# Kernel tuning notes

Measured on AMD Instinct MI355X. Metric: run time of the kernel, lower is better.

## Reference

```python
import jax, jax.numpy as jnp
import numpy as np

N, E, F, ED, L = 50000, 800000, 64, 16, 2
EPS_BN = 1e-5


def setup_inputs() -> dict:
    key = jax.random.key(0)
    ks = jax.random.split(key, 8)
    s = 0.05
    return {
        "x": jax.random.normal(ks[0], (N, F), jnp.float32),
        "edge_index": jax.random.randint(ks[1], (2, E), 0, N),
        "edge_attr": jax.random.normal(ks[2], (E, ED), jnp.float32),
        # per-layer stacked params (L layers)
        "We": jax.random.normal(ks[3], (L, ED, F), jnp.float32) * s,
        "be": jnp.zeros((L, F), jnp.float32),
        "Wpre": jax.random.normal(ks[4], (L, 2 * F, F), jnp.float32) * s,
        "bpre": jnp.zeros((L, F), jnp.float32),
        "Wpost": jax.random.normal(ks[5], (L, 7 * F, F), jnp.float32) * s,
        "bpost": jnp.zeros((L, F), jnp.float32),
        "Wlin": jax.random.normal(ks[6], (L, F, F), jnp.float32) * s,
        "blin": jnp.zeros((L, F), jnp.float32),
        "gamma": jnp.ones((L, F), jnp.float32),
        "beta": jnp.zeros((L, F), jnp.float32),
    }


def _layer(x, src, dst, edge_attr, We, be, Wpre, bpre, Wpost, bpost, Wlin, blin, gamma, beta):
    # message: edge encoder + pre-MLP on cat(x_j, e)   [E, F]
    e = edge_attr @ We + be
    h = jnp.concatenate([x[src], e], axis=-1) @ Wpre + bpre
    # multi-aggregator segment reduce to target nodes (index = dst)
    cnt = jax.ops.segment_sum(jnp.ones(h.shape[0], h.dtype), dst, num_segments=N)
    safe_cnt = jnp.maximum(cnt, 1.0)
    mean = jax.ops.segment_sum(h, dst, num_segments=N) / safe_cnt[:, None]
    empty = (cnt == 0)[:, None]
    mn = jnp.where(empty, 0.0, jax.ops.segment_min(h, dst, num_segments=N))
    mx = jnp.where(empty, 0.0, jax.ops.segment_max(h, dst, num_segments=N))
    agg = jnp.concatenate([mean, mn, mx], axis=-1)  # [N, 3F]
    # scalers: identity, then amplification (deg=None => avg from bincount of degrees)
    deg_i = cnt.astype(jnp.int32)
    bc = jnp.bincount(deg_i, length=N).astype(h.dtype)
    avg_log = jnp.mean(jnp.log(bc + 1.0))
    amp = (jnp.log(safe_cnt + 1.0) / avg_log)[:, None]
    out = jnp.concatenate([agg, agg * amp], axis=-1)  # [N, 6F]
    # post-MLP on cat(x, aggregated), final linear
    out = jnp.concatenate([x, out], axis=-1) @ Wpost + bpost  # [N, F]
    out = out @ Wlin + blin
    # BatchNorm1d (batch stats, biased var) + ReLU
    mu = out.mean(axis=0)
    var = jnp.mean((out - mu) ** 2, axis=0)
    out = gamma * (out - mu) / jnp.sqrt(var + EPS_BN) + beta
    return jax.nn.relu(out)


def reference(x, edge_index, edge_attr, We, be, Wpre, bpre, Wpost, bpost, Wlin, blin, gamma, beta):
    src, dst = edge_index[0], edge_index[1]
    for l in range(L):
        x = _layer(x, src, dst, edge_attr, We[l], be[l], Wpre[l], bpre[l],
                   Wpost[l], bpost[l], Wlin[l], blin[l], gamma[l], beta[l])
    return x
```

## Files before the change

kernel.cpp:

```cpp
#include <hip/hip_runtime.h>
#include <math.h>

static constexpr int NN = 50000;
static constexpr long NE = 800000;
static constexpr int FF = 64;
static constexpr int EDIM = 16;
static constexpr int NLAYER = 2;
static constexpr float EPSBN = 1e-5f;
static constexpr int NGRP = NN / 16;
static constexpr int SCB = 512;
static constexpr int NSCB = (NN + SCB - 1) / SCB;
static constexpr int LDSW = 68;

typedef __attribute__((ext_vector_type(8))) short short8v;
typedef __attribute__((ext_vector_type(4))) float f32x4;

#define MFMA16(a, b, c) __builtin_amdgcn_mfma_f32_16x16x32_bf16(a, b, c, 0, 0, 0)

__device__ __forceinline__ short f2bf(float f) {
    unsigned u = __float_as_uint(f);
    unsigned r = u + 0x7FFFu + ((u >> 16) & 1u);
    return (short)(r >> 16);
}
__device__ __forceinline__ float bf2f(unsigned short h) {
    return __uint_as_float(((unsigned)h) << 16);
}
__device__ __forceinline__ unsigned pk2(float lo, float hi) {
    return (unsigned)(unsigned short)f2bf(lo) | ((unsigned)(unsigned short)f2bf(hi) << 16);
}
__device__ __forceinline__ short8v pack8(const float* p) {
    const float4* q = (const float4*)p;
    float4 a = q[0], b = q[1];
    short8v v;
    v[0] = f2bf(a.x); v[1] = f2bf(a.y); v[2] = f2bf(a.z); v[3] = f2bf(a.w);
    v[4] = f2bf(b.x); v[5] = f2bf(b.y); v[6] = f2bf(b.z); v[7] = f2bf(b.w);
    return v;
}
__device__ __forceinline__ short8v pack8bn(const float* p, const float* sc, int f0) {
    const float4* q = (const float4*)p;
    float4 a = q[0], b = q[1];
    float v[8] = {a.x, a.y, a.z, a.w, b.x, b.y, b.z, b.w};
    short8v r;
#pragma unroll
    for (int j = 0; j < 8; ++j) {
        float y = fmaxf(fmaf(v[j], sc[f0 + j], sc[FF + f0 + j]), 0.f);
        r[j] = f2bf(y);
    }
    return r;
}
__device__ __forceinline__ void pack8s(const float* p, short8v& hi, short8v& lo) {
    const float4* q = (const float4*)p;
    float4 a = q[0], b = q[1];
    float v[8] = {a.x, a.y, a.z, a.w, b.x, b.y, b.z, b.w};
#pragma unroll
    for (int j = 0; j < 8; ++j) {
        short h = f2bf(v[j]);
        hi[j] = h;
        lo[j] = f2bf(v[j] - bf2f((unsigned short)h));
    }
}
__device__ __forceinline__ void pack8s_bn(const float* p, const float* sc, int f0,
                                          short8v& hi, short8v& lo) {
    const float4* q = (const float4*)p;
    float4 a = q[0], b = q[1];
    float v[8] = {a.x, a.y, a.z, a.w, b.x, b.y, b.z, b.w};
#pragma unroll
    for (int j = 0; j < 8; ++j) {
        float y = fmaxf(fmaf(v[j], sc[f0 + j], sc[FF + f0 + j]), 0.f);
        short h = f2bf(y);
        hi[j] = h;
        lo[j] = f2bf(y - bf2f((unsigned short)h));
    }
}
__device__ __forceinline__ void pack8fs(const float* v, short8v& hi, short8v& lo) {
#pragma unroll
    for (int j = 0; j < 8; ++j) {
        short h = f2bf(v[j]);
        hi[j] = h;
        lo[j] = f2bf(v[j] - bf2f((unsigned short)h));
    }
}

__global__ void fold_kernel(const float* __restrict__ We, const float* __restrict__ be,
                            const float* __restrict__ Wpre, const float* __restrict__ bpre,
                            const float* __restrict__ Wpost, const float* __restrict__ bpost,
                            const float* __restrict__ Wlin, const float* __restrict__ blin,
                            float* __restrict__ Weff, float* __restrict__ beff,
                            float* __restrict__ Wc, float* __restrict__ cfold) {
    int l = blockIdx.x >> 4;
    int s = blockIdx.x & 15;
    int t = threadIdx.x;
    const float* We_l    = We    + l * EDIM * FF;
    const float* Wpre_e  = Wpre  + l * 2 * FF * FF + FF * FF;
    const float* Wpost_l = Wpost + l * 7 * FF * FF;
    const float* Wlin_l  = Wlin  + l * FF * FF;

    __shared__ float slin[FF * FF];
    __shared__ float spre[FF * FF];
    for (int i = t; i < FF * FF; i += blockDim.x) { slin[i] = Wlin_l[i]; spre[i] = Wpre_e[i]; }
    __syncthreads();

    for (int i = s * 256 + t; i < EDIM * FF; i += 16 * 256) {
        int j = i >> 6, f = i & 63;
        float a = 0.f;
        for (int k = 0; k < FF; ++k) a += We_l[j * FF + k] * spre[k * FF + f];
        Weff[l * EDIM * FF + i] = a;
    }
    for (int i = s * 256 + t; i < FF; i += 16 * 256) {
        float a = bpre[l * FF + i];
        for (int k = 0; k < FF; ++k) a += be[l * FF + k] * spre[k * FF + i];
        beff[l * FF + i] = a;
    }
    for (int i = s * 256 + t; i < 7 * FF * FF; i += 16 * 256) {
        int r = i >> 6, f = i & 63;
        float a = 0.f;
        for (int k = 0; k < FF; ++k) a += Wpost_l[r * FF + k] * slin[k * FF + f];
        Wc[l * 7 * FF * FF + i] = a;
    }
    for (int i = s * 256 + t; i < FF; i += 16 * 256) {
        float a = blin[l * FF + i];
        for (int k = 0; k < FF; ++k) a += bpost[l * FF + k] * slin[k * FF + i];
        cfold[l * FF + i] = a;
    }
}

__global__ void fragify_all(const float* __restrict__ Wpre, const float* __restrict__ Weff,
                            const float* __restrict__ Wc,
                            short* __restrict__ WpreF, short* __restrict__ WeffF,
                            short* __restrict__ WcFh, short* __restrict__ WcFl) {
    int b = blockIdx.x;
    int l = b / 17, r = b % 17;
    int t = threadIdx.x;
    const float* src; short* dh; short* dl = nullptr; int kc, Kreal;
    if (r < 2)      { src = Wpre + (size_t)l * 2 * FF * FF; dh = WpreF + l * 4096;  kc = r;     Kreal = 64; }
    else if (r < 3) { src = Weff + (size_t)l * EDIM * FF;   dh = WeffF + l * 2048;  kc = 0;     Kreal = 16; }
    else            { src = Wc   + (size_t)l * 7 * FF * FF; dh = WcFh + l * 28672;
                      dl = WcFl + l * 28672;                                        kc = r - 3; Kreal = 448; }
    int idx = kc * 256 + t;
    int lane = idx & 63, nt = (idx >> 6) & 3;
    int m = lane & 15, kh = lane >> 4;
    short8v hv, lv;
#pragma unroll
    for (int j = 0; j < 8; ++j) {
        int k = kc * 32 + kh * 8 + j;
        float val = (k < Kreal) ? src[k * FF + nt * 16 + m] : 0.f;
        short h = f2bf(val);
        hv[j] = h;
        lv[j] = f2bf(val - bf2f((unsigned short)h));
    }
    ((short8v*)dh)[idx] = hv;
    if (dl) ((short8v*)dl)[idx] = lv;
}


__global__ void build_zero(int* __restrict__ rowcnt, int* __restrict__ fill,
                           int* __restrict__ bc, float* __restrict__ avglog) {
    long i = (long)blockIdx.x * 256 + threadIdx.x;
    long stride = (long)gridDim.x * 256;
    for (long j = i; j < NN; j += stride) { rowcnt[j] = 0; fill[j] = 0; bc[j] = 0; }
    if (i == 0) avglog[0] = 0.f;
}

__global__ void hist_dst(const int* __restrict__ ei, int* __restrict__ rowcnt) {
    long e = (long)blockIdx.x * 256 + threadIdx.x;
    if (e < NE) atomicAdd(&rowcnt[ei[NE + e]], 1);
}

__global__ void scan_a(const int* __restrict__ rowcnt, int* __restrict__ part) {
    __shared__ int red[SCB];
    int t = threadIdx.x;
    int i = blockIdx.x * SCB + t;
    red[t] = (i < NN) ? rowcnt[i] : 0;
    __syncthreads();
    for (int o = SCB / 2; o > 0; o >>= 1) {
        if (t < o) red[t] += red[t + o];
        __syncthreads();
    }
    if (t == 0) part[blockIdx.x] = red[0];
}

__global__ void scan_b(int* __restrict__ part, int* __restrict__ rowptr) {
    __shared__ int s[128];
    int t = threadIdx.x;
    int v = (t < NSCB) ? part[t] : 0;
    s[t] = v;
    __syncthreads();
    for (int o = 1; o < 128; o <<= 1) {
        int u = (t >= o) ? s[t - o] : 0;
        __syncthreads();
        s[t] += u;
        __syncthreads();
    }
    if (t < NSCB) part[t] = s[t] - v;
    if (t == 127) rowptr[NN] = s[127];
}

__global__ void scan_c(const int* __restrict__ rowcnt, const int* __restrict__ part,
                       int* __restrict__ rowptr) {
    __shared__ int s[SCB];
    int t = threadIdx.x;
    int i = blockIdx.x * SCB + t;
    int v = (i < NN) ? rowcnt[i] : 0;
    s[t] = v;
    __syncthreads();
    for (int o = 1; o < SCB; o <<= 1) {
        int u = (t >= o) ? s[t - o] : 0;
        __syncthreads();
        s[t] += u;
        __syncthreads();
    }
    if (i < NN) rowptr[i] = part[blockIdx.x] + s[t] - v;
}

__global__ void scatter_perm(const int* __restrict__ ei, const int* __restrict__ rowptr,
                             int* __restrict__ fill, int2* __restrict__ srcperm) {
    long e = (long)blockIdx.x * 256 + threadIdx.x;
    if (e >= NE) return;
    int d = ei[NE + e];
    int p = rowptr[d] + atomicAdd(&fill[d], 1);
    srcperm[p] = make_int2(ei[e], (int)e);
}

__global__ void gather_attr(const int2* __restrict__ srcperm, const float* __restrict__ attr,
                            int* __restrict__ srcp, short* __restrict__ attrb) {
    long p = (long)blockIdx.x * 256 + threadIdx.x;
    if (p >= NE) return;
    int2 sp = srcperm[p];
    srcp[p] = sp.x;
    long e = sp.y;
    const float4* a4 = (const float4*)(attr + e * EDIM);
    float4 A = a4[0], B = a4[1], C = a4[2], D = a4[3];
    uint4 w0, w1;
    w0.x = pk2(A.x, A.y); w0.y = pk2(A.z, A.w); w0.z = pk2(B.x, B.y); w0.w = pk2(B.z, B.w);
    w1.x = pk2(C.x, C.y); w1.y = pk2(C.z, C.w); w1.z = pk2(D.x, D.y); w1.w = pk2(D.z, D.w);
    uint4* dst = (uint4*)(attrb + p * EDIM);
    dst[0] = w0; dst[1] = w1;
}

__global__ void degbc2(const int* __restrict__ rowcnt, int* __restrict__ bc) {
    __shared__ int h[256];
    int t = threadIdx.x;
    h[t] = 0;
    __syncthreads();
    for (long n = (long)blockIdx.x * 256 + t; n < NN; n += (long)gridDim.x * 256) {
        int d = rowcnt[n];
        if (d < 256) {
            atomicAdd(&h[d], 1);
        } else {
            if (d >= NN) d = NN - 1;
            atomicAdd(&bc[d], 1);
        }
    }
    __syncthreads();
    int v = h[t];
    if (v) atomicAdd(&bc[t], v);
}

__global__ void avglog_kernel(const int* __restrict__ bc, float* __restrict__ total) {
    float s = 0.f;
    for (long i = (long)blockIdx.x * 256 + threadIdx.x; i < NN; i += (long)gridDim.x * 256)
        s += logf((float)bc[i] + 1.f);
    for (int o = 32; o; o >>= 1) s += __shfl_down(s, o, 64);
    __shared__ float wsum[4];
    int lane = threadIdx.x & 63, wid = threadIdx.x >> 6;
    if (lane == 0) wsum[wid] = s;
    __syncthreads();
    if (threadIdx.x == 0) atomicAdd(total, wsum[0] + wsum[1] + wsum[2] + wsum[3]);
}

__global__ void amp_kernel(const int* __restrict__ cnt, const float* __restrict__ total,
                           float* __restrict__ amp) {
    long n = (long)blockIdx.x * 256 + threadIdx.x;
    if (n < NN) {
        float avg = total[0] / (float)NN;
        float sc = fmaxf((float)cnt[n], 1.f);
        amp[n] = logf(sc + 1.f) / avg;
    }
}


__global__ __launch_bounds__(256) void xp_mfma(const float* __restrict__ xin,
                                               const float* __restrict__ bnsc,
                                               const short* __restrict__ WF,
                                               short* __restrict__ xpb,
                                               float* __restrict__ bnsum,
                                               float* __restrict__ bnsum2) {
    int t = threadIdx.x;
    if (blockIdx.x == 0 && t < FF) { bnsum[t] = 0.f; bnsum2[t] = 0.f; }
    int g = blockIdx.x * 4 + (t >> 6);
    if (g >= NGRP) return;
    int lane = t & 63, m = lane & 15, kh = lane >> 4;
    const float* xr = xin + (long)(g * 16 + m) * FF;
    short8v a0, a1;
    if (bnsc) {
        a0 = pack8bn(xr + kh * 8, bnsc, kh * 8);
        a1 = pack8bn(xr + 32 + kh * 8, bnsc, 32 + kh * 8);
    } else {
        a0 = pack8(xr + kh * 8);
        a1 = pack8(xr + 32 + kh * 8);
    }
    const short8v* BF = (const short8v*)WF;
    f32x4 acc[4];
#pragma unroll
    for (int nt = 0; nt < 4; ++nt) {
        f32x4 z = {0.f, 0.f, 0.f, 0.f};
        z = MFMA16(a0, BF[(0 * 4 + nt) * 64 + lane], z);
        z = MFMA16(a1, BF[(1 * 4 + nt) * 64 + lane], z);
        acc[nt] = z;
    }
#pragma unroll
    for (int nt = 0; nt < 4; ++nt)
#pragma unroll
        for (int r = 0; r < 4; ++r) {
            long node = g * 16 + kh * 4 + r;
            xpb[node * FF + nt * 16 + m] = f2bf(acc[nt][r]);
        }
}

__global__ __launch_bounds__(256) void agg_fused(
    const int* __restrict__ rowptr, const int* __restrict__ srcp,
    const short* __restrict__ attrb, const short* __restrict__ WF,
    const float* __restrict__ beff_l, const short* __restrict__ xpb,
    float* __restrict__ meanb, float* __restrict__ mnb, float* __restrict__ mxb) {
    __shared__ float eph[4][16 * LDSW];
    int t = threadIdx.x;
    int wid = t >> 6, lane = t & 63;
    int m = lane & 15, kh = lane >> 4;
    int n = blockIdx.x * 4 + wid;
    if (n >= NN) return;
    float* lds = &eph[wid][0];
    const short8v* BF = (const short8v*)WF;
    float bfv[4];
#pragma unroll
    for (int nt = 0; nt < 4; ++nt) bfv[nt] = beff_l[nt * 16 + m];
    long r0 = rowptr[n], r1 = rowptr[n + 1];
    const float INF = __builtin_huge_valf();
    float sm = 0.f, mn = INF, mx = -INF;
    const unsigned short* xu = (const unsigned short*)xpb;

    for (long base = r0; base < r1; base += 16) {
        int cnt = (int)(((r1 - base) < 16) ? (r1 - base) : 16);
        long ea = base + m; if (ea > NE - 1) ea = NE - 1;
        short8v a;
        if (kh < 2) {
            a = *(const short8v*)(attrb + ea * EDIM + kh * 8);
        } else {
#pragma unroll
            for (int j = 0; j < 8; ++j) a[j] = 0;
        }
        f32x4 ac0, ac1, ac2, ac3;
        {
            f32x4 z = {0.f, 0.f, 0.f, 0.f};
            ac0 = MFMA16(a, BF[0 * 64 + lane], z);
            ac1 = MFMA16(a, BF[1 * 64 + lane], z);
            ac2 = MFMA16(a, BF[2 * 64 + lane], z);
            ac3 = MFMA16(a, BF[3 * 64 + lane], z);
        }
#pragma unroll
        for (int r = 0; r < 4; ++r) {
            lds[(kh * 4 + r) * LDSW + 0 * 16 + m] = ac0[r] + bfv[0];
            lds[(kh * 4 + r) * LDSW + 1 * 16 + m] = ac1[r] + bfv[1];
            lds[(kh * 4 + r) * LDSW + 2 * 16 + m] = ac2[r] + bfv[2];
            lds[(kh * 4 + r) * LDSW + 3 * 16 + m] = ac3[r] + bfv[3];
        }
        int sv = srcp[base + (lane < cnt ? lane : cnt - 1)];
        int j = 0;
        for (; j + 8 <= cnt; j += 8) {
            int s0 = __shfl(sv, j + 0), s1 = __shfl(sv, j + 1);
            int s2 = __shfl(sv, j + 2), s3 = __shfl(sv, j + 3);
            int s4 = __shfl(sv, j + 4), s5 = __shfl(sv, j + 5);
            int s6 = __shfl(sv, j + 6), s7 = __shfl(sv, j + 7);
            float x0 = bf2f(xu[(long)s0 * FF + lane]);
            float x1 = bf2f(xu[(long)s1 * FF + lane]);
            float x2 = bf2f(xu[(long)s2 * FF + lane]);
            float x3 = bf2f(xu[(long)s3 * FF + lane]);
            float x4 = bf2f(xu[(long)s4 * FF + lane]);
            float x5 = bf2f(xu[(long)s5 * FF + lane]);
            float x6 = bf2f(xu[(long)s6 * FF + lane]);
            float x7 = bf2f(xu[(long)s7 * FF + lane]);
            float h0 = x0 + lds[(j + 0) * LDSW + lane];
            float h1 = x1 + lds[(j + 1) * LDSW + lane];
            float h2 = x2 + lds[(j + 2) * LDSW + lane];
            float h3 = x3 + lds[(j + 3) * LDSW + lane];
            float h4 = x4 + lds[(j + 4) * LDSW + lane];
            float h5 = x5 + lds[(j + 5) * LDSW + lane];
            float h6 = x6 + lds[(j + 6) * LDSW + lane];
            float h7 = x7 + lds[(j + 7) * LDSW + lane];
            sm += ((h0 + h1) + (h2 + h3)) + ((h4 + h5) + (h6 + h7));
            mn = fminf(mn, fminf(fminf(fminf(h0, h1), fminf(h2, h3)),
                                 fminf(fminf(h4, h5), fminf(h6, h7))));
            mx = fmaxf(mx, fmaxf(fmaxf(fmaxf(h0, h1), fmaxf(h2, h3)),
                                 fmaxf(fmaxf(h4, h5), fmaxf(h6, h7))));
        }
        for (; j < cnt; ++j) {
            int s0 = __shfl(sv, j);
            float h = bf2f(xu[(long)s0 * FF + lane]) + lds[j * LDSW + lane];
            sm += h;
            mn = fminf(mn, h);
            mx = fmaxf(mx, h);
        }
    }
    int deg = (int)(r1 - r0);
    float inv = (deg > 0) ? (1.f / (float)deg) : 0.f;
    if (deg == 0) { mn = 0.f; mx = 0.f; }
    long o = (long)n * FF + lane;
    meanb[o] = sm * inv; mnb[o] = mn; mxb[o] = mx;
}

__global__ __launch_bounds__(256, 2) void node_mfma(
    const float* __restrict__ xin, const float* __restrict__ bnsc,
    const float* __restrict__ meanb, const float* __restrict__ mnb,
    const float* __restrict__ mxb, const float* __restrict__ amp,
    const short* __restrict__ WFh, const short* __restrict__ WFl,
    const float* __restrict__ cfold_l,
    float* __restrict__ out_pre, float* __restrict__ bnsum, float* __restrict__ bnsum2) {
    __shared__ float sS[FF], sQ[FF];
    int t = threadIdx.x;
    if (t < FF) { sS[t] = 0.f; sQ[t] = 0.f; }
    __syncthreads();
    int g = blockIdx.x * 4 + (t >> 6);
    bool act = (g < NGRP);
    int lane = t & 63, m = lane & 15, kh = lane >> 4;
    if (act) {
        long n = g * 16 + m;
        float av = amp[n];
        const float* xr = xin + n * FF;
        float vme[16], vmn[16], vmx[16], sc16[16];
        {
            const float4* s4a = (const float4*)(meanb + n * FF + kh * 8);
            const float4* s4b = (const float4*)(meanb + n * FF + 32 + kh * 8);
            float4 a = s4a[0], b = s4a[1], c = s4b[0], d = s4b[1];
            vme[0]=a.x; vme[1]=a.y; vme[2]=a.z; vme[3]=a.w;
            vme[4]=b.x; vme[5]=b.y; vme[6]=b.z; vme[7]=b.w;
            vme[8]=c.x; vme[9]=c.y; vme[10]=c.z; vme[11]=c.w;
            vme[12]=d.x; vme[13]=d.y; vme[14]=d.z; vme[15]=d.w;
        }
        {
            const float4* s4a = (const float4*)(mnb + n * FF + kh * 8);
            const float4* s4b = (const float4*)(mnb + n * FF + 32 + kh * 8);
            float4 a = s4a[0], b = s4a[1], c = s4b[0], d = s4b[1];
            vmn[0]=a.x; vmn[1]=a.y; vmn[2]=a.z; vmn[3]=a.w;
            vmn[4]=b.x; vmn[5]=b.y; vmn[6]=b.z; vmn[7]=b.w;
            vmn[8]=c.x; vmn[9]=c.y; vmn[10]=c.z; vmn[11]=c.w;
            vmn[12]=d.x; vmn[13]=d.y; vmn[14]=d.z; vmn[15]=d.w;
        }
        {
            const float4* s4a = (const float4*)(mxb + n * FF + kh * 8);
            const float4* s4b = (const float4*)(mxb + n * FF + 32 + kh * 8);
            float4 a = s4a[0], b = s4a[1], c = s4b[0], d = s4b[1];
            vmx[0]=a.x; vmx[1]=a.y; vmx[2]=a.z; vmx[3]=a.w;
            vmx[4]=b.x; vmx[5]=b.y; vmx[6]=b.z; vmx[7]=b.w;
            vmx[8]=c.x; vmx[9]=c.y; vmx[10]=c.z; vmx[11]=c.w;
            vmx[12]=d.x; vmx[13]=d.y; vmx[14]=d.z; vmx[15]=d.w;
        }
        const short8v* BH = (const short8v*)WFh;
        const short8v* BL = (const short8v*)WFl;
        f32x4 accA[4], accB[4];
#pragma unroll
        for (int nt = 0; nt < 4; ++nt) {
            f32x4 z = {0.f, 0.f, 0.f, 0.f};
            accA[nt] = z; accB[nt] = z;
        }
        short8v hv, lv;
#define DO_KC3(kc, ACC) { \
        _Pragma("unroll") for (int nt = 0; nt < 4; ++nt) { \
            ACC[nt] = MFMA16(hv, BH[((kc) * 4 + nt) * 64 + lane], ACC[nt]); \
            ACC[nt] = MFMA16(lv, BH[((kc) * 4 + nt) * 64 + lane], ACC[nt]); \
            ACC[nt] = MFMA16(hv, BL[((kc) * 4 + nt) * 64 + lane], ACC[nt]); } }
        if (bnsc) {
            pack8s_bn(xr + kh * 8, bnsc, kh * 8, hv, lv);           DO_KC3(0, accA)
            pack8s_bn(xr + 32 + kh * 8, bnsc, 32 + kh * 8, hv, lv); DO_KC3(1, accB)
        } else {
            pack8s(xr + kh * 8, hv, lv);        DO_KC3(0, accA)
            pack8s(xr + 32 + kh * 8, hv, lv);   DO_KC3(1, accB)
        }
        pack8fs(vme + 0, hv, lv);           DO_KC3(2, accA)
        pack8fs(vme + 8, hv, lv);           DO_KC3(3, accB)
        pack8fs(vmn + 0, hv, lv);           DO_KC3(4, accA)
        pack8fs(vmn + 8, hv, lv);           DO_KC3(5, accB)
        pack8fs(vmx + 0, hv, lv);           DO_KC3(6, accA)
        pack8fs(vmx + 8, hv, lv);           DO_KC3(7, accB)
#pragma unroll
        for (int j = 0; j < 16; ++j) sc16[j] = vme[j] * av;
        pack8fs(sc16 + 0, hv, lv);          DO_KC3(8, accA)
        pack8fs(sc16 + 8, hv, lv);          DO_KC3(9, accB)
#pragma unroll
        for (int j = 0; j < 16; ++j) sc16[j] = vmn[j] * av;
        pack8fs(sc16 + 0, hv, lv);          DO_KC3(10, accA)
        pack8fs(sc16 + 8, hv, lv);          DO_KC3(11, accB)
#pragma unroll
        for (int j = 0; j < 16; ++j) sc16[j] = vmx[j] * av;
        pack8fs(sc16 + 0, hv, lv);          DO_KC3(12, accA)
        pack8fs(sc16 + 8, hv, lv);          DO_KC3(13, accB)
#undef DO_KC3
        float cfv[4];
#pragma unroll
        for (int nt = 0; nt < 4; ++nt) cfv[nt] = cfold_l[nt * 16 + m];
#pragma unroll
        for (int nt = 0; nt < 4; ++nt) {
            float ps = 0.f, pq = 0.f;
#pragma unroll
            for (int r = 0; r < 4; ++r) {
                float v = accA[nt][r] + accB[nt][r] + cfv[nt];
                out_pre[(long)(g * 16 + kh * 4 + r) * FF + nt * 16 + m] = v;
                ps += v;
                pq += v * v;
            }
            atomicAdd(&sS[nt * 16 + m], ps);
            atomicAdd(&sQ[nt * 16 + m], pq);
        }
    }
    __syncthreads();
    if (t < FF) {
        atomicAdd(&bnsum[t], sS[t]);
        atomicAdd(&bnsum2[t], sQ[t]);
    }
}

__global__ void bn_final(const float* __restrict__ bnsum, const float* __restrict__ bnsum2,
                         const float* __restrict__ gamma_l, const float* __restrict__ beta_l,
                         float* __restrict__ sc_sh) {
    int f = threadIdx.x;
    if (f < FF) {
        float mu = bnsum[f] / (float)NN;
        float var = bnsum2[f] / (float)NN - mu * mu;
        var = fmaxf(var, 0.f);
        float s = gamma_l[f] * rsqrtf(var + EPSBN);
        sc_sh[f] = s;
        sc_sh[FF + f] = beta_l[f] - mu * s;
    }
}

__global__ void bn_apply2(const float* __restrict__ out_pre,
                          const float* __restrict__ bnsum, const float* __restrict__ bnsum2,
                          const float* __restrict__ gamma_l, const float* __restrict__ beta_l,
                          float* __restrict__ xout) {
    int f = threadIdx.x & 63;
    float mu = bnsum[f] / (float)NN;
    float var = bnsum2[f] / (float)NN - mu * mu;
    var = fmaxf(var, 0.f);
    float s = gamma_l[f] * rsqrtf(var + EPSBN);
    float o = beta_l[f] - mu * s;
    long i = (long)blockIdx.x * 256 + threadIdx.x;
    long stride = (long)gridDim.x * 256;
    for (long j = i; j < (long)NN * FF; j += stride) {
        xout[j] = fmaxf(fmaf(out_pre[j], s, o), 0.f);
    }
}

extern "C" void kernel_launch(void* const* d_in, const int* in_sizes, int n_in,
                              void* d_out, int out_size, void* d_ws, size_t ws_size,
                              hipStream_t stream) {
    const float* x0    = (const float*)d_in[0];
    const int*   ei    = (const int*)d_in[1];
    const float* attr  = (const float*)d_in[2];
    const float* We    = (const float*)d_in[3];
    const float* be    = (const float*)d_in[4];
    const float* Wpre  = (const float*)d_in[5];
    const float* bpre  = (const float*)d_in[6];
    const float* Wpost = (const float*)d_in[7];
    const float* bpost = (const float*)d_in[8];
    const float* Wlin  = (const float*)d_in[9];
    const float* blin  = (const float*)d_in[10];
    const float* gamma = (const float*)d_in[11];
    const float* beta  = (const float*)d_in[12];
    float* out = (float*)d_out;

    char* ws = (char*)d_ws;
    size_t off = 0;
    auto carve = [&](size_t bytes) -> void* {
        void* p = ws + off;
        off += (bytes + 255) & ~(size_t)255;
        return p;
    };
    const size_t NFb = (size_t)NN * FF * 4;
    float*    Weff   = (float*)carve(2 * EDIM * FF * 4);
    float*    beff   = (float*)carve(2 * FF * 4);
    float*    Wc     = (float*)carve(2 * 7 * FF * FF * 4);
    float*    cfold  = (float*)carve(2 * FF * 4);
    short*    WpreF  = (short*)carve(2 * 4096 * 2);
    short*    WeffF  = (short*)carve(2 * 2048 * 2);
    short*    WcFh   = (short*)carve(2 * 28672 * 2);
    short*    WcFl   = (short*)carve(2 * 28672 * 2);
    int*      srcp   = (int*)carve(NE * 4);
    short*    attrb  = (short*)carve((size_t)NE * EDIM * 2);
    int*      rowptr = (int*)carve((NN + 1) * 4);
    int*      rowcnt = (int*)carve(NN * 4);
    int*      fill   = (int*)carve(NN * 4);
    int*      bc     = (int*)carve(NN * 4);
    float*    amp    = (float*)carve(NN * 4);
    int*      part   = (int*)carve(NSCB * 4);
    short*    xpb    = (short*)carve((size_t)NN * FF * 2);
    float*    meanb  = (float*)carve(NFb);
    float*    mnb    = (float*)carve(NFb);
    float*    mxb    = (float*)carve(NFb);
    float*    preA   = (float*)carve(NFb);
    float*    preB   = (float*)carve(NFb);
    float*    bnsum  = (float*)carve(FF * 4);
    float*    bnsum2 = (float*)carve(FF * 4);
    float*    avglog = (float*)carve(4);
    float*    sc_sh  = (float*)carve(2 * FF * 4);
    int2*     srcperm = (int2*)preB;

    const int EB = (int)((NE + 255) / 256);

    build_zero<<<196, 256, 0, stream>>>(rowcnt, fill, bc, avglog);
    hist_dst<<<EB, 256, 0, stream>>>(ei, rowcnt);
    scan_a<<<NSCB, SCB, 0, stream>>>(rowcnt, part);
    scan_b<<<1, 128, 0, stream>>>(part, rowptr);
    scan_c<<<NSCB, SCB, 0, stream>>>(rowcnt, part, rowptr);
    scatter_perm<<<EB, 256, 0, stream>>>(ei, rowptr, fill, srcperm);
    gather_attr<<<EB, 256, 0, stream>>>(srcperm, attr, srcp, attrb);
    degbc2<<<196, 256, 0, stream>>>(rowcnt, bc);
    avglog_kernel<<<128, 256, 0, stream>>>(bc, avglog);
    amp_kernel<<<196, 256, 0, stream>>>(rowcnt, avglog, amp);
    fold_kernel<<<32, 256, 0, stream>>>(We, be, Wpre, bpre, Wpost, bpost, Wlin, blin,
                                        Weff, beff, Wc, cfold);
    fragify_all<<<34, 256, 0, stream>>>(Wpre, Weff, Wc, WpreF, WeffF, WcFh, WcFl);

    for (int l = 0; l < NLAYER; ++l) {
        const float* xin  = (l == 0) ? x0 : ((l & 1) ? preA : preB);
        const float* bnsc = (l == 0) ? nullptr : sc_sh;
        float* pre        = (l & 1) ? preB : preA;

        xp_mfma<<<(NGRP + 3) / 4, 256, 0, stream>>>(xin, bnsc, WpreF + l * 4096, xpb,
                                                    bnsum, bnsum2);
        agg_fused<<<12500, 256, 0, stream>>>(rowptr, srcp, attrb, WeffF + l * 2048,
                                             beff + l * FF, xpb, meanb, mnb, mxb);
        node_mfma<<<(NGRP + 3) / 4, 256, 0, stream>>>(xin, bnsc, meanb, mnb, mxb, amp,
                                                      WcFh + l * 28672, WcFl + l * 28672,
                                                      cfold + l * FF,
                                                      pre, bnsum, bnsum2);
        if (l < NLAYER - 1)
            bn_final<<<1, 64, 0, stream>>>(bnsum, bnsum2, gamma + l * FF, beta + l * FF, sc_sh);
        else
            bn_apply2<<<4096, 256, 0, stream>>>(pre, bnsum, bnsum2,
                                                gamma + l * FF, beta + l * FF, out);
    }
}
```

Baseline: 353.6 us.

## Make node MLP kernel persistent with LDS-resident half weights and replicated BN sums

The node post-MLP kernel becomes a persistent grid of 512 blocks. Each block handles half of the 64 output columns and stages that half of the hi/lo bf16 weight fragments (about 57 KB) in LDS once, then loops over node groups with a stride. BatchNorm partial sums build up in registers across the loop and are flushed into 8 replicated global accumulators. The bn kernels sum those replicas before use. This removes repeated global weight fetches and global atomic contention, at the cost of reading every input row twice (once per column half) and lower occupancy from the large LDS footprint.

```diff
diff --git a/kernel.cpp b/kernel.cpp
--- a/kernel.cpp
+++ b/kernel.cpp
@@ -283,10 +283,11 @@
                                                const float* __restrict__ bnsc,
                                                const short* __restrict__ WF,
                                                short* __restrict__ xpb,
-                                               float* __restrict__ bnsum,
-                                               float* __restrict__ bnsum2) {
-    int t = threadIdx.x;
-    if (blockIdx.x == 0 && t < FF) { bnsum[t] = 0.f; bnsum2[t] = 0.f; }
+                                               float* __restrict__ bnsumR) {
+    int t = threadIdx.x;
+    if (blockIdx.x == 0) {
+        for (int i = t; i < 1024; i += 256) bnsumR[i] = 0.f;
+    }
     int g = blockIdx.x * 4 + (t >> 6);
     if (g >= NGRP) return;
     int lane = t & 63, m = lane & 15, kh = lane >> 4;
@@ -407,22 +408,41 @@
     meanb[o] = sm * inv; mnb[o] = mn; mxb[o] = mx;
 }
 
-__global__ __launch_bounds__(256, 2) void node_mfma(
+__global__ __launch_bounds__(256, 2) void node_mfma3(
     const float* __restrict__ xin, const float* __restrict__ bnsc,
     const float* __restrict__ meanb, const float* __restrict__ mnb,
     const float* __restrict__ mxb, const float* __restrict__ amp,
     const short* __restrict__ WFh, const short* __restrict__ WFl,
     const float* __restrict__ cfold_l,
-    float* __restrict__ out_pre, float* __restrict__ bnsum, float* __restrict__ bnsum2) {
-    __shared__ float sS[FF], sQ[FF];
-    int t = threadIdx.x;
-    if (t < FF) { sS[t] = 0.f; sQ[t] = 0.f; }
-    __syncthreads();
-    int g = blockIdx.x * 4 + (t >> 6);
-    bool act = (g < NGRP);
+    float* __restrict__ out_pre, float* __restrict__ bnsumR) {
+    __shared__ short wlds[2 * 14336];
+    __shared__ float sS[32], sQ[32];
+    int t = threadIdx.x;
+    int half = blockIdx.x & 1;
     int lane = t & 63, m = lane & 15, kh = lane >> 4;
-    if (act) {
-        long n = g * 16 + m;
+    {
+        const short8v* gh = (const short8v*)WFh;
+        const short8v* gl = (const short8v*)WFl;
+        short8v* dh = (short8v*)wlds;
+        short8v* dl = (short8v*)(wlds + 14336);
+        for (int i = t; i < 1792; i += 256) {
+            int fl = i >> 6, ln = i & 63;
+            int kc = fl >> 1, ntl = fl & 1;
+            int fg = (kc * 4 + half * 2 + ntl) * 64 + ln;
+            dh[i] = gh[fg];
+            dl[i] = gl[fg];
+        }
+    }
+    if (t < 32) { sS[t] = 0.f; sQ[t] = 0.f; }
+    __syncthreads();
+    const short8v* BH = (const short8v*)wlds;
+    const short8v* BL = (const short8v*)(wlds + 14336);
+    float cf0 = cfold_l[(half * 2 + 0) * 16 + m];
+    float cf1 = cfold_l[(half * 2 + 1) * 16 + m];
+    float bs0 = 0.f, bq0 = 0.f, bs1 = 0.f, bq1 = 0.f;
+
+    for (int g = (int)(blockIdx.x >> 1) * 4 + (t >> 6); g < NGRP; g += 1024) {
+        long n = (long)g * 16 + m;
         float av = amp[n];
         const float* xr = xin + n * FF;
         float vme[16], vmn[16], vmx[16], sc16[16];
@@ -453,98 +473,107 @@
             vmx[8]=c.x; vmx[9]=c.y; vmx[10]=c.z; vmx[11]=c.w;
             vmx[12]=d.x; vmx[13]=d.y; vmx[14]=d.z; vmx[15]=d.w;
         }
-        const short8v* BH = (const short8v*)WFh;
-        const short8v* BL = (const short8v*)WFl;
-        f32x4 accA[4], accB[4];
-#pragma unroll
-        for (int nt = 0; nt < 4; ++nt) {
+        f32x4 aA0, aB0, aA1, aB1;
+        {
             f32x4 z = {0.f, 0.f, 0.f, 0.f};
-            accA[nt] = z; accB[nt] = z;
+            aA0 = z; aB0 = z; aA1 = z; aB1 = z;
         }
         short8v hv, lv;
-#define DO_KC3(kc, ACC) { \
-        _Pragma("unroll") for (int nt = 0; nt < 4; ++nt) { \
-            ACC[nt] = MFMA16(hv, BH[((kc) * 4 + nt) * 64 + lane], ACC[nt]); \
-            ACC[nt] = MFMA16(lv, BH[((kc) * 4 + nt) * 64 + lane], ACC[nt]); \
-            ACC[nt] = MFMA16(hv, BL[((kc) * 4 + nt) * 64 + lane], ACC[nt]); } }
+#define DO3(kc, X0, X1) { \
+        X0 = MFMA16(hv, BH[((kc) * 2 + 0) * 64 + lane], X0); \
+        X0 = MFMA16(lv, BH[((kc) * 2 + 0) * 64 + lane], X0); \
+        X0 = MFMA16(hv, BL[((kc) * 2 + 0) * 64 + lane], X0); \
+        X1 = MFMA16(hv, BH[((kc) * 2 + 1) * 64 + lane], X1); \
+        X1 = MFMA16(lv, BH[((kc) * 2 + 1) * 64 + lane], X1); \
+        X1 = MFMA16(hv, BL[((kc) * 2 + 1) * 64 + lane], X1); }
         if (bnsc) {
-            pack8s_bn(xr + kh * 8, bnsc, kh * 8, hv, lv);           DO_KC3(0, accA)
-            pack8s_bn(xr + 32 + kh * 8, bnsc, 32 + kh * 8, hv, lv); DO_KC3(1, accB)
+            pack8s_bn(xr + kh * 8, bnsc, kh * 8, hv, lv);           DO3(0, aA0, aA1)
+            pack8s_bn(xr + 32 + kh * 8, bnsc, 32 + kh * 8, hv, lv); DO3(1, aB0, aB1)
         } else {
-            pack8s(xr + kh * 8, hv, lv);        DO_KC3(0, accA)
-            pack8s(xr + 32 + kh * 8, hv, lv);   DO_KC3(1, accB)
-        }
-        pack8fs(vme + 0, hv, lv);           DO_KC3(2, accA)
-        pack8fs(vme + 8, hv, lv);           DO_KC3(3, accB)
-        pack8fs(vmn + 0, hv, lv);           DO_KC3(4, accA)
-        pack8fs(vmn + 8, hv, lv);           DO_KC3(5, accB)
-        pack8fs(vmx + 0, hv, lv);           DO_KC3(6, accA)
-        pack8fs(vmx + 8, hv, lv);           DO_KC3(7, accB)
+            pack8s(xr + kh * 8, hv, lv);        DO3(0, aA0, aA1)
+            pack8s(xr + 32 + kh * 8, hv, lv);   DO3(1, aB0, aB1)
+        }
+        pack8fs(vme + 0, hv, lv);           DO3(2, aA0, aA1)
+        pack8fs(vme + 8, hv, lv);           DO3(3, aB0, aB1)
+        pack8fs(vmn + 0, hv, lv);           DO3(4, aA0, aA1)
+        pack8fs(vmn + 8, hv, lv);           DO3(5, aB0, aB1)
+        pack8fs(vmx + 0, hv, lv);           DO3(6, aA0, aA1)
+        pack8fs(vmx + 8, hv, lv);           DO3(7, aB0, aB1)
 #pragma unroll
         for (int j = 0; j < 16; ++j) sc16[j] = vme[j] * av;
-        pack8fs(sc16 + 0, hv, lv);          DO_KC3(8, accA)
-        pack8fs(sc16 + 8, hv, lv);          DO_KC3(9, accB)
+        pack8fs(sc16 + 0, hv, lv);          DO3(8, aA0, aA1)
+        pack8fs(sc16 + 8, hv, lv);          DO3(9, aB0, aB1)
 #pragma unroll
         for (int j = 0; j < 16; ++j) sc16[j] = vmn[j] * av;
-        pack8fs(sc16 + 0, hv, lv);          DO_KC3(10, accA)
-        pack8fs(sc16 + 8, hv, lv);          DO_KC3(11, accB)
+        pack8fs(sc16 + 0, hv, lv);          DO3(10, aA0, aA1)
+        pack8fs(sc16 + 8, hv, lv);          DO3(11, aB0, aB1)
 #pragma unroll
         for (int j = 0; j < 16; ++j) sc16[j] = vmx[j] * av;
-        pack8fs(sc16 + 0, hv, lv);          DO_KC3(12, accA)
-        pack8fs(sc16 + 8, hv, lv);          DO_KC3(13, accB)
-#undef DO_KC3
-        float cfv[4];
-#pragma unroll
-        for (int nt = 0; nt < 4; ++nt) cfv[nt] = cfold_l[nt * 16 + m];
-#pragma unroll
-        for (int nt = 0; nt < 4; ++nt) {
-            float ps = 0.f, pq = 0.f;
-#pragma unroll
-            for (int r = 0; r < 4; ++r) {
-                float v = accA[nt][r] + accB[nt][r] + cfv[nt];
-                out_pre[(long)(g * 16 + kh * 4 + r) * FF + nt * 16 + m] = v;
-                ps += v;
-                pq += v * v;
-            }
-            atomicAdd(&sS[nt * 16 + m], ps);
-            atomicAdd(&sQ[nt * 16 + m], pq);
-        }
-    }
-    __syncthreads();
-    if (t < FF) {
-        atomicAdd(&bnsum[t], sS[t]);
-        atomicAdd(&bnsum2[t], sQ[t]);
-    }
-}
-
-__global__ void bn_final(const float* __restrict__ bnsum, const float* __restrict__ bnsum2,
+        pack8fs(sc16 + 0, hv, lv);          DO3(12, aA0, aA1)
+        pack8fs(sc16 + 8, hv, lv);          DO3(13, aB0, aB1)
+#undef DO3
+#pragma unroll
+        for (int r = 0; r < 4; ++r) {
+            long row = ((long)g * 16 + kh * 4 + r) * FF;
+            float v0 = aA0[r] + aB0[r] + cf0;
+            float v1 = aA1[r] + aB1[r] + cf1;
+            out_pre[row + (half * 2 + 0) * 16 + m] = v0;
+            out_pre[row + (half * 2 + 1) * 16 + m] = v1;
+            bs0 += v0; bq0 += v0 * v0;
+            bs1 += v1; bq1 += v1 * v1;
+        }
+    }
+    atomicAdd(&sS[m], bs0);       atomicAdd(&sQ[m], bq0);
+    atomicAdd(&sS[16 + m], bs1);  atomicAdd(&sQ[16 + m], bq1);
+    __syncthreads();
+    if (t < 32) {
+        int rep = (int)(blockIdx.x >> 1) & 7;
+        int f = half * 32 + t;
+        atomicAdd(&bnsumR[rep * 64 + f], sS[t]);
+        atomicAdd(&bnsumR[512 + rep * 64 + f], sQ[t]);
+    }
+}
+
+__global__ void bn_final(const float* __restrict__ bnsumR,
                          const float* __restrict__ gamma_l, const float* __restrict__ beta_l,
                          float* __restrict__ sc_sh) {
     int f = threadIdx.x;
     if (f < FF) {
-        float mu = bnsum[f] / (float)NN;
-        float var = bnsum2[f] / (float)NN - mu * mu;
+        float s = 0.f, q = 0.f;
+#pragma unroll
+        for (int r = 0; r < 8; ++r) {
+            s += bnsumR[r * 64 + f];
+            q += bnsumR[512 + r * 64 + f];
+        }
+        float mu = s / (float)NN;
+        float var = q / (float)NN - mu * mu;
         var = fmaxf(var, 0.f);
-        float s = gamma_l[f] * rsqrtf(var + EPSBN);
-        sc_sh[f] = s;
-        sc_sh[FF + f] = beta_l[f] - mu * s;
+        float sc = gamma_l[f] * rsqrtf(var + EPSBN);
+        sc_sh[f] = sc;
+        sc_sh[FF + f] = beta_l[f] - mu * sc;
     }
 }
 
 __global__ void bn_apply2(const float* __restrict__ out_pre,
-                          const float* __restrict__ bnsum, const float* __restrict__ bnsum2,
+                          const float* __restrict__ bnsumR,
                           const float* __restrict__ gamma_l, const float* __restrict__ beta_l,
                           float* __restrict__ xout) {
     int f = threadIdx.x & 63;
-    float mu = bnsum[f] / (float)NN;
-    float var = bnsum2[f] / (float)NN - mu * mu;
+    float s = 0.f, q = 0.f;
+#pragma unroll
+    for (int r = 0; r < 8; ++r) {
+        s += bnsumR[r * 64 + f];
+        q += bnsumR[512 + r * 64 + f];
+    }
+    float mu = s / (float)NN;
+    float var = q / (float)NN - mu * mu;
     var = fmaxf(var, 0.f);
-    float s = gamma_l[f] * rsqrtf(var + EPSBN);
-    float o = beta_l[f] - mu * s;
+    float sc = gamma_l[f] * rsqrtf(var + EPSBN);
+    float o = beta_l[f] - mu * sc;
     long i = (long)blockIdx.x * 256 + threadIdx.x;
     long stride = (long)gridDim.x * 256;
     for (long j = i; j < (long)NN * FF; j += stride) {
-        xout[j] = fmaxf(fmaf(out_pre[j], s, o), 0.f);
+        xout[j] = fmaxf(fmaf(out_pre[j], sc, o), 0.f);
     }
 }
 
@@ -596,8 +625,7 @@
     float*    mxb    = (float*)carve(NFb);
     float*    preA   = (float*)carve(NFb);
     float*    preB   = (float*)carve(NFb);
-    float*    bnsum  = (float*)carve(FF * 4);
-    float*    bnsum2 = (float*)carve(FF * 4);
+    float*    bnsumR = (float*)carve(1024 * 4);
     float*    avglog = (float*)carve(4);
     float*    sc_sh  = (float*)carve(2 * FF * 4);
     int2*     srcperm = (int2*)preB;
@@ -623,18 +651,16 @@
         const float* bnsc = (l == 0) ? nullptr : sc_sh;
         float* pre        = (l & 1) ? preB : preA;
 
-        xp_mfma<<<(NGRP + 3) / 4, 256, 0, stream>>>(xin, bnsc, WpreF + l * 4096, xpb,
-                                                    bnsum, bnsum2);
+        xp_mfma<<<(NGRP + 3) / 4, 256, 0, stream>>>(xin, bnsc, WpreF + l * 4096, xpb, bnsumR);
         agg_fused<<<12500, 256, 0, stream>>>(rowptr, srcp, attrb, WeffF + l * 2048,
                                              beff + l * FF, xpb, meanb, mnb, mxb);
-        node_mfma<<<(NGRP + 3) / 4, 256, 0, stream>>>(xin, bnsc, meanb, mnb, mxb, amp,
-                                                      WcFh + l * 28672, WcFl + l * 28672,
-                                                      cfold + l * FF,
-                                                      pre, bnsum, bnsum2);
+        node_mfma3<<<512, 256, 0, stream>>>(xin, bnsc, meanb, mnb, mxb, amp,
+                                            WcFh + l * 28672, WcFl + l * 28672,
+                                            cfold + l * FF, pre, bnsumR);
         if (l < NLAYER - 1)
-            bn_final<<<1, 64, 0, stream>>>(bnsum, bnsum2, gamma + l * FF, beta + l * FF, sc_sh);
+            bn_final<<<1, 64, 0, stream>>>(bnsumR, gamma + l * FF, beta + l * FF, sc_sh);
         else
-            bn_apply2<<<4096, 256, 0, stream>>>(pre, bnsum, bnsum2,
+            bn_apply2<<<4096, 256, 0, stream>>>(pre, bnsumR,
                                                 gamma + l * FF, beta + l * FF, out);
     }
 }
```

New measurement: 357.1 us. No clear change (+1.0%).

## Stage node-MLP weight fragments in LDS with persistent blocks and replicated BN sums

Applied to the files above, without the earlier changes.

The node MLP kernel becomes a persistent kernel of 256 blocks with 512 threads each. Each block copies the hi/lo bf16 weight fragments (about 112 KB) into dynamic LDS once, then loops over node groups, so the MFMA B operands are no longer re-read from global/L2 for every group. BatchNorm partial sums are kept in registers across the loop and flushed once per block into 8 replicated global slots, which cuts global atomic contention. In exchange, occupancy drops to one large block per CU, each block pays an upfront LDS fill, and the wide LDS reads may hit bank conflicts.

```diff
diff --git a/kernel.cpp b/kernel.cpp
--- a/kernel.cpp
+++ b/kernel.cpp
@@ -11,6 +11,8 @@
 static constexpr int SCB = 512;
 static constexpr int NSCB = (NN + SCB - 1) / SCB;
 static constexpr int LDSW = 68;
+static constexpr int WFRAG = 28672;
+static constexpr size_t NODE_LDS = (size_t)WFRAG * 2 * 2 + 512;
 
 typedef __attribute__((ext_vector_type(8))) short short8v;
 typedef __attribute__((ext_vector_type(4))) float f32x4;
@@ -134,8 +136,8 @@
     const float* src; short* dh; short* dl = nullptr; int kc, Kreal;
     if (r < 2)      { src = Wpre + (size_t)l * 2 * FF * FF; dh = WpreF + l * 4096;  kc = r;     Kreal = 64; }
     else if (r < 3) { src = Weff + (size_t)l * EDIM * FF;   dh = WeffF + l * 2048;  kc = 0;     Kreal = 16; }
-    else            { src = Wc   + (size_t)l * 7 * FF * FF; dh = WcFh + l * 28672;
-                      dl = WcFl + l * 28672;                                        kc = r - 3; Kreal = 448; }
+    else            { src = Wc   + (size_t)l * 7 * FF * FF; dh = WcFh + l * WFRAG;
+                      dl = WcFl + l * WFRAG;                                        kc = r - 3; Kreal = 448; }
     int idx = kc * 256 + t;
     int lane = idx & 63, nt = (idx >> 6) & 3;
     int m = lane & 15, kh = lane >> 4;
@@ -283,10 +285,11 @@
                                                const float* __restrict__ bnsc,
                                                const short* __restrict__ WF,
                                                short* __restrict__ xpb,
-                                               float* __restrict__ bnsum,
-                                               float* __restrict__ bnsum2) {
-    int t = threadIdx.x;
-    if (blockIdx.x == 0 && t < FF) { bnsum[t] = 0.f; bnsum2[t] = 0.f; }
+                                               float* __restrict__ bnsumR) {
+    int t = threadIdx.x;
+    if (blockIdx.x == 0) {
+        for (int i = t; i < 1024; i += 256) bnsumR[i] = 0.f;
+    }
     int g = blockIdx.x * 4 + (t >> 6);
     if (g >= NGRP) return;
     int lane = t & 63, m = lane & 15, kh = lane >> 4;
@@ -407,22 +410,39 @@
     meanb[o] = sm * inv; mnb[o] = mn; mxb[o] = mx;
 }
 
-__global__ __launch_bounds__(256, 2) void node_mfma(
+__global__ __launch_bounds__(512, 1) void node_mfma5(
     const float* __restrict__ xin, const float* __restrict__ bnsc,
     const float* __restrict__ meanb, const float* __restrict__ mnb,
     const float* __restrict__ mxb, const float* __restrict__ amp,
     const short* __restrict__ WFh, const short* __restrict__ WFl,
     const float* __restrict__ cfold_l,
-    float* __restrict__ out_pre, float* __restrict__ bnsum, float* __restrict__ bnsum2) {
-    __shared__ float sS[FF], sQ[FF];
-    int t = threadIdx.x;
-    if (t < FF) { sS[t] = 0.f; sQ[t] = 0.f; }
-    __syncthreads();
-    int g = blockIdx.x * 4 + (t >> 6);
-    bool act = (g < NGRP);
-    int lane = t & 63, m = lane & 15, kh = lane >> 4;
-    if (act) {
-        long n = g * 16 + m;
+    float* __restrict__ out_pre, float* __restrict__ bnsumR) {
+    extern __shared__ short wlds[];
+    float* sS = (float*)(wlds + 2 * WFRAG);
+    float* sQ = sS + 64;
+    int t = threadIdx.x;
+    int w = t >> 6, lane = t & 63, m = lane & 15, kh = lane >> 4;
+    {
+        const short8v* gh = (const short8v*)WFh;
+        const short8v* gl = (const short8v*)WFl;
+        short8v* dh = (short8v*)wlds;
+        short8v* dl = (short8v*)(wlds + WFRAG);
+        for (int i = t; i < WFRAG / 8; i += 512) {
+            dh[i] = gh[i];
+            dl[i] = gl[i];
+        }
+    }
+    if (t < 64) { sS[t] = 0.f; sQ[t] = 0.f; }
+    __syncthreads();
+    const short8v* BH = (const short8v*)wlds;
+    const short8v* BL = (const short8v*)(wlds + WFRAG);
+    float cfv[4];
+#pragma unroll
+    for (int nt = 0; nt < 4; ++nt) cfv[nt] = cfold_l[nt * 16 + m];
+    float bs[4] = {0.f, 0.f, 0.f, 0.f}, bq[4] = {0.f, 0.f, 0.f, 0.f};
+
+    for (int g = blockIdx.x * 8 + w; g < NGRP; g += 2048) {
+        long n = (long)g * 16 + m;
         float av = amp[n];
         const float* xr = xin + n * FF;
         float vme[16], vmn[16], vmx[16], sc16[16];
@@ -453,8 +473,6 @@
             vmx[8]=c.x; vmx[9]=c.y; vmx[10]=c.z; vmx[11]=c.w;
             vmx[12]=d.x; vmx[13]=d.y; vmx[14]=d.z; vmx[15]=d.w;
         }
-        const short8v* BH = (const short8v*)WFh;
-        const short8v* BL = (const short8v*)WFl;
         f32x4 accA[4], accB[4];
 #pragma unroll
         for (int nt = 0; nt < 4; ++nt) {
@@ -493,58 +511,73 @@
         pack8fs(sc16 + 0, hv, lv);          DO_KC3(12, accA)
         pack8fs(sc16 + 8, hv, lv);          DO_KC3(13, accB)
 #undef DO_KC3
-        float cfv[4];
-#pragma unroll
-        for (int nt = 0; nt < 4; ++nt) cfv[nt] = cfold_l[nt * 16 + m];
 #pragma unroll
         for (int nt = 0; nt < 4; ++nt) {
             float ps = 0.f, pq = 0.f;
 #pragma unroll
             for (int r = 0; r < 4; ++r) {
                 float v = accA[nt][r] + accB[nt][r] + cfv[nt];
-                out_pre[(long)(g * 16 + kh * 4 + r) * FF + nt * 16 + m] = v;
+                out_pre[((long)g * 16 + kh * 4 + r) * FF + nt * 16 + m] = v;
                 ps += v;
                 pq += v * v;
             }
-            atomicAdd(&sS[nt * 16 + m], ps);
-            atomicAdd(&sQ[nt * 16 + m], pq);
-        }
-    }
-    __syncthreads();
-    if (t < FF) {
-        atomicAdd(&bnsum[t], sS[t]);
-        atomicAdd(&bnsum2[t], sQ[t]);
-    }
-}
-
-__global__ void bn_final(const float* __restrict__ bnsum, const float* __restrict__ bnsum2,
+            bs[nt] += ps;
+            bq[nt] += pq;
+        }
+    }
+#pragma unroll
+    for (int nt = 0; nt < 4; ++nt) {
+        atomicAdd(&sS[nt * 16 + m], bs[nt]);
+        atomicAdd(&sQ[nt * 16 + m], bq[nt]);
+    }
+    __syncthreads();
+    if (t < 64) {
+        int rep = blockIdx.x & 7;
+        atomicAdd(&bnsumR[rep * 64 + t], sS[t]);
+        atomicAdd(&bnsumR[512 + rep * 64 + t], sQ[t]);
+    }
+}
+
+__global__ void bn_final(const float* __restrict__ bnsumR,
                          const float* __restrict__ gamma_l, const float* __restrict__ beta_l,
                          float* __restrict__ sc_sh) {
     int f = threadIdx.x;
     if (f < FF) {
-        float mu = bnsum[f] / (float)NN;
-        float var = bnsum2[f] / (float)NN - mu * mu;
+        float s = 0.f, q = 0.f;
+#pragma unroll
+        for (int r = 0; r < 8; ++r) {
+            s += bnsumR[r * 64 + f];
+            q += bnsumR[512 + r * 64 + f];
+        }
+        float mu = s / (float)NN;
+        float var = q / (float)NN - mu * mu;
         var = fmaxf(var, 0.f);
-        float s = gamma_l[f] * rsqrtf(var + EPSBN);
-        sc_sh[f] = s;
-        sc_sh[FF + f] = beta_l[f] - mu * s;
+        float sc = gamma_l[f] * rsqrtf(var + EPSBN);
+        sc_sh[f] = sc;
+        sc_sh[FF + f] = beta_l[f] - mu * sc;
     }
 }
 
 __global__ void bn_apply2(const float* __restrict__ out_pre,
-                          const float* __restrict__ bnsum, const float* __restrict__ bnsum2,
+                          const float* __restrict__ bnsumR,
                           const float* __restrict__ gamma_l, const float* __restrict__ beta_l,
                           float* __restrict__ xout) {
     int f = threadIdx.x & 63;
-    float mu = bnsum[f] / (float)NN;
-    float var = bnsum2[f] / (float)NN - mu * mu;
+    float s = 0.f, q = 0.f;
+#pragma unroll
+    for (int r = 0; r < 8; ++r) {
+        s += bnsumR[r * 64 + f];
+        q += bnsumR[512 + r * 64 + f];
+    }
+    float mu = s / (float)NN;
+    float var = q / (float)NN - mu * mu;
     var = fmaxf(var, 0.f);
-    float s = gamma_l[f] * rsqrtf(var + EPSBN);
-    float o = beta_l[f] - mu * s;
+    float sc = gamma_l[f] * rsqrtf(var + EPSBN);
+    float o = beta_l[f] - mu * sc;
     long i = (long)blockIdx.x * 256 + threadIdx.x;
     long stride = (long)gridDim.x * 256;
     for (long j = i; j < (long)NN * FF; j += stride) {
-        xout[j] = fmaxf(fmaf(out_pre[j], s, o), 0.f);
+        xout[j] = fmaxf(fmaf(out_pre[j], sc, o), 0.f);
     }
 }
 
@@ -566,6 +599,9 @@
     const float* beta  = (const float*)d_in[12];
     float* out = (float*)d_out;
 
+    hipFuncSetAttribute((const void*)node_mfma5,
+                        hipFuncAttributeMaxDynamicSharedMemorySize, (int)NODE_LDS);
+
     char* ws = (char*)d_ws;
     size_t off = 0;
     auto carve = [&](size_t bytes) -> void* {
@@ -580,8 +616,8 @@
     float*    cfold  = (float*)carve(2 * FF * 4);
     short*    WpreF  = (short*)carve(2 * 4096 * 2);
     short*    WeffF  = (short*)carve(2 * 2048 * 2);
-    short*    WcFh   = (short*)carve(2 * 28672 * 2);
-    short*    WcFl   = (short*)carve(2 * 28672 * 2);
+    short*    WcFh   = (short*)carve(2 * WFRAG * 2);
+    short*    WcFl   = (short*)carve(2 * WFRAG * 2);
     int*      srcp   = (int*)carve(NE * 4);
     short*    attrb  = (short*)carve((size_t)NE * EDIM * 2);
     int*      rowptr = (int*)carve((NN + 1) * 4);
@@ -596,8 +632,7 @@
     float*    mxb    = (float*)carve(NFb);
     float*    preA   = (float*)carve(NFb);
     float*    preB   = (float*)carve(NFb);
-    float*    bnsum  = (float*)carve(FF * 4);
-    float*    bnsum2 = (float*)carve(FF * 4);
+    float*    bnsumR = (float*)carve(1024 * 4);
     float*    avglog = (float*)carve(4);
     float*    sc_sh  = (float*)carve(2 * FF * 4);
     int2*     srcperm = (int2*)preB;
@@ -623,18 +658,16 @@
         const float* bnsc = (l == 0) ? nullptr : sc_sh;
         float* pre        = (l & 1) ? preB : preA;
 
-        xp_mfma<<<(NGRP + 3) / 4, 256, 0, stream>>>(xin, bnsc, WpreF + l * 4096, xpb,
-                                                    bnsum, bnsum2);
+        xp_mfma<<<(NGRP + 3) / 4, 256, 0, stream>>>(xin, bnsc, WpreF + l * 4096, xpb, bnsumR);
         agg_fused<<<12500, 256, 0, stream>>>(rowptr, srcp, attrb, WeffF + l * 2048,
                                              beff + l * FF, xpb, meanb, mnb, mxb);
-        node_mfma<<<(NGRP + 3) / 4, 256, 0, stream>>>(xin, bnsc, meanb, mnb, mxb, amp,
-                                                      WcFh + l * 28672, WcFl + l * 28672,
-                                                      cfold + l * FF,
-                                                      pre, bnsum, bnsum2);
+        node_mfma5<<<256, 512, NODE_LDS, stream>>>(xin, bnsc, meanb, mnb, mxb, amp,
+                                                   WcFh + l * WFRAG, WcFl + l * WFRAG,
+                                                   cfold + l * FF, pre, bnsumR);
         if (l < NLAYER - 1)
-            bn_final<<<1, 64, 0, stream>>>(bnsum, bnsum2, gamma + l * FF, beta + l * FF, sc_sh);
+            bn_final<<<1, 64, 0, stream>>>(bnsumR, gamma + l * FF, beta + l * FF, sc_sh);
         else
-            bn_apply2<<<4096, 256, 0, stream>>>(pre, bnsum, bnsum2,
+            bn_apply2<<<4096, 256, 0, stream>>>(pre, bnsumR,
                                                 gamma + l * FF, beta + l * FF, out);
     }
 }
```

After: 457.3 us. +29.3%, slower.
